# Performance work log

Measured on AMD Instinct MI355X. Metric: run time of the kernel, lower is better.

The kernel has to match this reference:

```python
import jax, jax.numpy as jnp
import numpy as np

N_FFT = 2048
HOP = 512
K = N_FFT // 2 + 1  # 1025 output frequency bins


def _dft_window_weights(n_fft):
    """Windowed real/imag DFT matrices, matching librosa hann (periodic) window
    and W[j,k] = exp(-2*pi*i*j*k/n_fft); conv weight = (W[:, :K] * win[:, None]).T."""
    n = np.arange(n_fft)
    win = 0.5 - 0.5 * np.cos(2.0 * np.pi * n / n_fft)  # hann, fftbins=True
    k = np.arange(n_fft // 2 + 1)
    ang = 2.0 * np.pi * np.outer(k, n) / n_fft  # (K, n_fft)
    w_real = np.cos(ang) * win[None, :]
    w_imag = -np.sin(ang) * win[None, :]
    return (jnp.asarray(w_real, jnp.float32), jnp.asarray(w_imag, jnp.float32))


def setup_inputs() -> dict:
    key = jax.random.key(0)
    x = jax.random.normal(key, (16, 2, 262144), dtype=jnp.float32)
    w_real, w_imag = _dft_window_weights(N_FFT)
    return {"x": x, "w_real": w_real, "w_imag": w_imag}


def reference(x, w_real, w_imag):
    B, C, L = x.shape
    pad = N_FFT // 2
    xp = jnp.pad(x, ((0, 0), (0, 0), (pad, pad)), mode="reflect")  # center=True
    T = (L + 2 * pad - N_FFT) // HOP + 1  # number of frames
    idx = HOP * jnp.arange(T)[:, None] + jnp.arange(N_FFT)[None, :]  # (T, n_fft)
    frames = xp[:, :, idx]  # (B, C, T, n_fft)
    # Windowed DFT as GEMM (same math as the conv-as-DFT in the torch module).
    real = jnp.einsum("bctn,kn->bckt", frames, w_real)  # (B, C, K, T)
    imag = jnp.einsum("bctn,kn->bckt", frames, w_imag)
    # torch.cat over channel dim -> (B, C*K, T), channel-major order
    real = real.reshape(B, C * K, T)
    imag = imag.reshape(B, C * K, T)
    return (real, imag)
```

## Files before the change

### kernel.cpp

```cpp
#include <hip/hip_runtime.h>
#include <hip/hip_fp16.h>

#define NFFT  2048
#define KF    1025
#define MROWS 2050
#define TT    513
#define HOPS  512
#define LSIG  262144
#define PADL  1024
#define XPADN 264192
#define XDN   66048
#define IMOFF (16 * MROWS * TT)
#define NBC   32

typedef __attribute__((ext_vector_type(8))) short bf16x8;
typedef __attribute__((ext_vector_type(4))) short bf16x4;
typedef __attribute__((ext_vector_type(4))) float f32x4;

__device__ __forceinline__ short f2bf(float f) {
    union { float f; unsigned u; } v; v.f = f;
    unsigned r = v.u + 0x7fffu + ((v.u >> 16) & 1u);
    return (short)(r >> 16);
}

typedef __attribute__((address_space(1))) void gas_void;
typedef __attribute__((address_space(3))) void las_void;

__device__ __forceinline__ void gload_lds16(const short* g, short* l) {
    __builtin_amdgcn_global_load_lds((gas_void*)(void*)const_cast<short*>(g),
                                     (las_void*)(void*)l, 16, 0, 0);
}

__global__ __launch_bounds__(256)
void prep_x(const float* __restrict__ x, short* __restrict__ xpad,
            short* __restrict__ xd) {
    const int bc = blockIdx.y;
    const int j4 = (blockIdx.x * 256 + threadIdx.x) * 4;
    const float* xb = x + (size_t)bc * LSIG;
    float4 v;
    if (j4 >= PADL && j4 + 4 <= PADL + LSIG) {
        v = *(const float4*)(xb + (j4 - PADL));
    } else {
        float t[4];
#pragma unroll
        for (int e = 0; e < 4; e++) {
            int s = j4 + e - PADL;
            if (s < 0) s = -s;
            if (s >= LSIG) s = 2 * LSIG - 2 - s;
            t[e] = xb[s];
        }
        v = make_float4(t[0], t[1], t[2], t[3]);
    }
    bf16x4 b = { f2bf(v.x), f2bf(v.y), f2bf(v.z), f2bf(v.w) };
    *(bf16x4*)(xpad + (size_t)bc * XPADN + j4) = b;
    const int j = j4 >> 2;
#pragma unroll
    for (int r = 0; r < 4; r++)
        xd[((size_t)r * NBC + bc) * XDN + j] = b[r];
}

__global__ __launch_bounds__(256)
void prep_basis(short* __restrict__ A) {
    const int r    = blockIdx.y;
    const int row  = blockIdx.x;
    const int kap  = row >> 1;
    const int reim = row & 1;
    for (int m = threadIdx.x; m < 512; m += 256) {
        float sv, cv;
        sincospif((float)(kap * m) * (1.0f / 256.0f), &sv, &cv);
        float win = 0.5f - 0.5f * cospif((float)(4 * m + r) * (1.0f / 1024.0f));
        float val = reim ? (-win * sv) : (win * cv);
        A[((size_t)r * 512 + row) * 512 + m] = f2bf(val);
    }
}

__global__ __launch_bounds__(256)
void stft_gemm_s(const short* __restrict__ Ab, const short* __restrict__ xd,
                 __half* __restrict__ S, int bc0) {
    __shared__ short As[128 * 64];
    __shared__ short Bs[128 * 64];

    const int tid   = threadIdx.x;
    const int bcl   = blockIdx.x;
    const int r     = blockIdx.y >> 2;
    const int mBase = (blockIdx.y & 3) * 128;
    const int t0    = blockIdx.z * 128;
    const short* Ap  = Ab + (size_t)r * 512 * 512;
    const short* xdp = xd + ((size_t)r * NBC + (bc0 + bcl)) * XDN;

    const int lane = tid & 63;
    const int wid  = tid >> 6;
    const int wm   = (wid >> 1) * 64;
    const int wn   = (wid & 1) * 64;
    const int l16  = lane & 15;
    const int quad = lane >> 4;

    const int lrow = lane >> 3;
    const int csrc = (lane & 7) ^ lrow;
    const int rb   = 32 * wid;

    const short* srcA[4]; const short* srcB[4];
    short* dstA[4]; short* dstB[4];
#pragma unroll
    for (int i = 0; i < 4; i++) {
        int rr = rb + 8 * i + lrow;
        srcA[i] = Ap  + (size_t)(mBase + rr) * 512 + csrc * 8;
        srcB[i] = xdp + (size_t)(t0 + rr) * 128 + csrc * 8;
        dstA[i] = As + (rb + 8 * i) * 64;
        dstB[i] = Bs + (rb + 8 * i) * 64;
    }

    f32x4 acc[4][4];
#pragma unroll
    for (int i = 0; i < 4; i++)
#pragma unroll
        for (int j = 0; j < 4; j++)
            acc[i][j] = (f32x4){0.f, 0.f, 0.f, 0.f};

    const int r7 = l16 & 7;
    for (int kt = 0; kt < 512; kt += 64) {
        __syncthreads();
#pragma unroll
        for (int i = 0; i < 4; i++) {
            gload_lds16(srcA[i] + kt, dstA[i]);
            gload_lds16(srcB[i] + kt, dstB[i]);
        }
        __syncthreads();
#pragma unroll
        for (int kk = 0; kk < 64; kk += 32) {
            const int p = ((kk >> 5) * 4 + quad) ^ r7;
            bf16x8 af[4], bfr[4];
#pragma unroll
            for (int i = 0; i < 4; i++)
                af[i] = *(const bf16x8*)(As + (wm + i * 16 + l16) * 64 + p * 8);
#pragma unroll
            for (int j = 0; j < 4; j++)
                bfr[j] = *(const bf16x8*)(Bs + (wn + j * 16 + l16) * 64 + p * 8);
#pragma unroll
            for (int i = 0; i < 4; i++)
#pragma unroll
                for (int j = 0; j < 4; j++)
                    acc[i][j] = __builtin_amdgcn_mfma_f32_16x16x32_bf16(
                        af[i], bfr[j], acc[i][j], 0, 0, 0);
        }
    }

    __half* Sb = S + ((size_t)bcl * 4 + r) * (512 * 512);
#pragma unroll
    for (int i = 0; i < 4; i++) {
#pragma unroll
        for (int rr = 0; rr < 4; rr++) {
            int row = mBase + wm + i * 16 + quad * 4 + rr;
            int tc  = t0 + wn + l16;
#pragma unroll
            for (int j = 0; j < 4; j++)
                Sb[(size_t)row * 512 + tc + j * 16] = __float2half(acc[i][j][rr]);
        }
    }
}

__global__ __launch_bounds__(256)
void stft_combine(const __half* __restrict__ S, float* __restrict__ out, int bc0) {
    const int kap = blockIdx.x;
    const int bcl = blockIdx.y;
    const int bcg = bc0 + bcl;
    float s1, c1;
    sincospif((float)kap * (1.0f / 1024.0f), &s1, &c1);
    const float cr1 = c1,               ci1 = -s1;
    const float cr2 = cr1*cr1 - ci1*ci1, ci2 = 2.f*cr1*ci1;
    const float cr3 = cr2*cr1 - ci2*ci1, ci3 = cr2*ci1 + ci2*cr1;
    const __half* Sb = S + (size_t)bcl * 4 * 512 * 512;
    float* oRe = out + (size_t)bcg * KF * TT;
    float* oIm = out + IMOFF + (size_t)bcg * KF * TT;

#pragma unroll
    for (int ti = 0; ti < 2; ti++) {
        const int t = threadIdx.x + ti * 256;
        float a[4], b[4];
#pragma unroll
        for (int r = 0; r < 4; r++) {
            a[r] = __half2float(Sb[((size_t)r * 512 + 2 * kap) * 512 + t]);
            b[r] = __half2float(Sb[((size_t)r * 512 + 2 * kap + 1) * 512 + t]);
        }
        const float u0 = a[0], v0 = b[0];
        const float u1 = cr1*a[1] - ci1*b[1], v1 = cr1*b[1] + ci1*a[1];
        const float u2 = cr2*a[2] - ci2*b[2], v2 = cr2*b[2] + ci2*a[2];
        const float u3 = cr3*a[3] - ci3*b[3], v3 = cr3*b[3] + ci3*a[3];
        oRe[(size_t)kap * TT + t]          = u0 + u1 + u2 + u3;
        oIm[(size_t)kap * TT + t]          = v0 + v1 + v2 + v3;
        oRe[(size_t)(kap + 512) * TT + t]  = u0 + v1 - u2 - v3;
        oIm[(size_t)(kap + 512) * TT + t]  = v0 - u1 - v2 + u3;
        oRe[(size_t)(512 - kap) * TT + t]  = u0 - v1 - u2 + v3;
        oIm[(size_t)(512 - kap) * TT + t]  = -(v0 + u1 - v2 - u3);
        oRe[(size_t)(1024 - kap) * TT + t] = u0 - u1 + u2 - u3;
        oIm[(size_t)(1024 - kap) * TT + t] = -(v0 - v1 + v2 - v3);
    }
}

__global__ __launch_bounds__(256)
void stft_tail(const float* __restrict__ wr, const float* __restrict__ wi,
               const short* __restrict__ xpad, float* __restrict__ out) {
    const int bx   = blockIdx.x;
    const int tid  = threadIdx.x;
    const int lane = tid & 63;
    const int wid  = tid >> 6;
    const int l16  = lane & 15;
    const int quad = lane >> 4;

    if (bx < 17) {
        const int mBase = bx * 128 + wid * 32;
        f32x4 acc[2][2];
#pragma unroll
        for (int i = 0; i < 2; i++)
#pragma unroll
            for (int j = 0; j < 2; j++) acc[i][j] = (f32x4){0.f,0.f,0.f,0.f};
        int ra0 = min(mBase + l16, MROWS - 1);
        int ra1 = min(mBase + 16 + l16, MROWS - 1);
        const float* a0p = ((ra0 < KF) ? (wr + (size_t)ra0 * NFFT)
                                       : (wi + (size_t)(ra0 - KF) * NFFT)) + quad * 8;
        const float* a1p = ((ra1 < KF) ? (wr + (size_t)ra1 * NFFT)
                                       : (wi + (size_t)(ra1 - KF) * NFFT)) + quad * 8;
        const short* b0p = xpad + (size_t)l16 * XPADN + LSIG + quad * 8;
        const short* b1p = b0p + (size_t)16 * XPADN;
        for (int kt = 0; kt < NFFT; kt += 32) {
            float4 f0 = *(const float4*)(a0p + kt), f1 = *(const float4*)(a0p + kt + 4);
            float4 g0 = *(const float4*)(a1p + kt), g1 = *(const float4*)(a1p + kt + 4);
            bf16x8 a0 = { f2bf(f0.x), f2bf(f0.y), f2bf(f0.z), f2bf(f0.w),
                          f2bf(f1.x), f2bf(f1.y), f2bf(f1.z), f2bf(f1.w) };
            bf16x8 a1 = { f2bf(g0.x), f2bf(g0.y), f2bf(g0.z), f2bf(g0.w),
                          f2bf(g1.x), f2bf(g1.y), f2bf(g1.z), f2bf(g1.w) };
            bf16x8 b0 = *(const bf16x8*)(b0p + kt);
            bf16x8 b1 = *(const bf16x8*)(b1p + kt);
            acc[0][0] = __builtin_amdgcn_mfma_f32_16x16x32_bf16(a0, b0, acc[0][0], 0,0,0);
            acc[0][1] = __builtin_amdgcn_mfma_f32_16x16x32_bf16(a0, b1, acc[0][1], 0,0,0);
            acc[1][0] = __builtin_amdgcn_mfma_f32_16x16x32_bf16(a1, b0, acc[1][0], 0,0,0);
            acc[1][1] = __builtin_amdgcn_mfma_f32_16x16x32_bf16(a1, b1, acc[1][1], 0,0,0);
        }
#pragma unroll
        for (int i = 0; i < 2; i++)
#pragma unroll
            for (int j = 0; j < 2; j++)
#pragma unroll
                for (int rr = 0; rr < 4; rr++) {
                    int row = mBase + i * 16 + quad * 4 + rr;
                    if (row >= MROWS) continue;
                    int bc = j * 16 + l16;
                    size_t o = (row < KF)
                        ? ((size_t)(bc * KF + row) * TT + (TT - 1))
                        : (IMOFF + (size_t)(bc * KF + (row - KF)) * TT + (TT - 1));
                    out[o] = acc[i][j][rr];
                }
    } else {
        const int idx = bx - 17;
        const int bc  = idx >> 3;
        const int tb  = idx & 7;
        const int t0  = (tb * 4 + wid) * 16;
        const int ls  = l16 & 3;
        const int k   = 256 + (ls & 1) * 512;
        const float* bp = ((ls & 2) ? wi : wr) + (size_t)k * NFFT + quad * 8;
        const short* ap = xpad + (size_t)bc * XPADN + (size_t)(t0 + l16) * HOPS + quad * 8;
        f32x4 acc0 = {0.f,0.f,0.f,0.f}, acc1 = {0.f,0.f,0.f,0.f};
        for (int kt = 0; kt < NFFT; kt += 64) {
            bf16x8 a0 = *(const bf16x8*)(ap + kt);
            bf16x8 a1 = *(const bf16x8*)(ap + kt + 32);
            float4 f0 = *(const float4*)(bp + kt), f1 = *(const float4*)(bp + kt + 4);
            float4 g0 = *(const float4*)(bp + kt + 32), g1 = *(const float4*)(bp + kt + 36);
            bf16x8 b0 = { f2bf(f0.x), f2bf(f0.y), f2bf(f0.z), f2bf(f0.w),
                          f2bf(f1.x), f2bf(f1.y), f2bf(f1.z), f2bf(f1.w) };
            bf16x8 b1 = { f2bf(g0.x), f2bf(g0.y), f2bf(g0.z), f2bf(g0.w),
                          f2bf(g1.x), f2bf(g1.y), f2bf(g1.z), f2bf(g1.w) };
            acc0 = __builtin_amdgcn_mfma_f32_16x16x32_bf16(a0, b0, acc0, 0,0,0);
            acc1 = __builtin_amdgcn_mfma_f32_16x16x32_bf16(a1, b1, acc1, 0,0,0);
        }
        if (l16 < 4) {
            size_t base = ((ls & 2) ? (size_t)IMOFF : 0) + (size_t)(bc * KF + k) * TT;
#pragma unroll
            for (int rr = 0; rr < 4; rr++) {
                int t = t0 + quad * 4 + rr;
                out[base + t] = acc0[rr] + acc1[rr];
            }
        }
    }
}

extern "C" void kernel_launch(void* const* d_in, const int* in_sizes, int n_in,
                              void* d_out, int out_size, void* d_ws, size_t ws_size,
                              hipStream_t stream) {
    const float* x  = (const float*)d_in[0];
    const float* wr = (const float*)d_in[1];
    const float* wi = (const float*)d_in[2];
    float* out = (float*)d_out;

    char* ws = (char*)d_ws;
    short*  xpad = (short*)ws;
    short*  xd   = (short*)(ws + 16908288);
    short*  Ab   = (short*)(ws + 33816576);
    __half* S    = (__half*)(ws + 35913728);

    const long long s_per_bc = 4LL * 512 * 512 * sizeof(__half);
    long long avail = (long long)ws_size - 35913728LL;
    int CH = (int)(avail / s_per_bc);
    if (CH < 1) CH = 1;
    if (CH > NBC) CH = NBC;

    prep_x<<<dim3(258, NBC), 256, 0, stream>>>(x, xpad, xd);
    prep_basis<<<dim3(512, 4), 256, 0, stream>>>(Ab);

    for (int bc0 = 0; bc0 < NBC; bc0 += CH) {
        int c = NBC - bc0 < CH ? NBC - bc0 : CH;
        stft_gemm_s<<<dim3(c, 16, 4), 256, 0, stream>>>(Ab, xd, S, bc0);
        stft_combine<<<dim3(256, c), 256, 0, stream>>>(S, out, bc0);
    }

    stft_tail<<<17 + 256, 256, 0, stream>>>(wr, wi, xpad, out);
}
```

Baseline: 321.2 us.

## Fuse radix-4 combine into GEMM epilogue, dropping fp16 intermediate buffer

The four polyphase sub-GEMMs are now computed in one kernel that keeps all four accumulator sets in registers. The radix-4 twiddle-free combine is applied in the epilogue, writing final fp32 outputs directly. This removes the fp16 S intermediate round trip through global memory, the separate combine kernel, and the chunking loop. The basis is now built from the provided weight tensors instead of sincos, and the last-frame tail is handled by extending the GEMM grid with clamped rows. In exchange the kernel uses more registers, with launch bounds set for 2 blocks per SM, and a smaller N tile, which may hurt reuse.

```diff
diff --git a/kernel.cpp b/kernel.cpp
--- a/kernel.cpp
+++ b/kernel.cpp
@@ -1,5 +1,4 @@
 #include <hip/hip_runtime.h>
-#include <hip/hip_fp16.h>
 
 #define NFFT  2048
 #define KF    1025
@@ -60,225 +59,165 @@
 }
 
 __global__ __launch_bounds__(256)
-void prep_basis(short* __restrict__ A) {
-    const int r    = blockIdx.y;
-    const int row  = blockIdx.x;
-    const int kap  = row >> 1;
-    const int reim = row & 1;
-    for (int m = threadIdx.x; m < 512; m += 256) {
-        float sv, cv;
-        sincospif((float)(kap * m) * (1.0f / 256.0f), &sv, &cv);
-        float win = 0.5f - 0.5f * cospif((float)(4 * m + r) * (1.0f / 1024.0f));
-        float val = reim ? (-win * sv) : (win * cv);
-        A[((size_t)r * 512 + row) * 512 + m] = f2bf(val);
-    }
-}
-
-__global__ __launch_bounds__(256)
-void stft_gemm_s(const short* __restrict__ Ab, const short* __restrict__ xd,
-                 __half* __restrict__ S, int bc0) {
-    __shared__ short As[128 * 64];
-    __shared__ short Bs[128 * 64];
+void prep_basis2(const float* __restrict__ wr, const float* __restrict__ wi,
+                 short* __restrict__ A) {
+    const int r   = blockIdx.y;
+    const int row = blockIdx.x;
+    const float* w = ((row & 1) ? wi : wr) + (size_t)(row >> 1) * NFFT + r;
+    short* dst = A + ((size_t)r * 512 + row) * 512;
+    for (int m = threadIdx.x; m < 512; m += 256)
+        dst[m] = f2bf(w[4 * m]);
+}
+
+__global__ __launch_bounds__(256, 2)
+void stft_gemm_f(const short* __restrict__ Ab, const short* __restrict__ xd,
+                 float* __restrict__ out) {
+    __shared__ short As[2][128 * 64];
+    __shared__ short Bs[2][64 * 64];
 
     const int tid   = threadIdx.x;
-    const int bcl   = blockIdx.x;
-    const int r     = blockIdx.y >> 2;
-    const int mBase = (blockIdx.y & 3) * 128;
-    const int t0    = blockIdx.z * 128;
-    const short* Ap  = Ab + (size_t)r * 512 * 512;
-    const short* xdp = xd + ((size_t)r * NBC + (bc0 + bcl)) * XDN;
+    const int bcg   = blockIdx.x;
+    const int mBase = blockIdx.y * 128;
+    const int t0    = blockIdx.z * 64;
 
     const int lane = tid & 63;
     const int wid  = tid >> 6;
     const int wm   = (wid >> 1) * 64;
-    const int wn   = (wid & 1) * 64;
+    const int wn   = (wid & 1) * 32;
     const int l16  = lane & 15;
     const int quad = lane >> 4;
 
     const int lrow = lane >> 3;
     const int csrc = (lane & 7) ^ lrow;
-    const int rb   = 32 * wid;
-
-    const short* srcA[4]; const short* srcB[4];
-    short* dstA[4]; short* dstB[4];
-#pragma unroll
-    for (int i = 0; i < 4; i++) {
-        int rr = rb + 8 * i + lrow;
-        srcA[i] = Ap  + (size_t)(mBase + rr) * 512 + csrc * 8;
-        srcB[i] = xdp + (size_t)(t0 + rr) * 128 + csrc * 8;
-        dstA[i] = As + (rb + 8 * i) * 64;
-        dstB[i] = Bs + (rb + 8 * i) * 64;
-    }
-
-    f32x4 acc[4][4];
-#pragma unroll
-    for (int i = 0; i < 4; i++)
-#pragma unroll
-        for (int j = 0; j < 4; j++)
-            acc[i][j] = (f32x4){0.f, 0.f, 0.f, 0.f};
+    const int rbA  = 32 * wid;
+    const int rbB  = 16 * wid;
+
+    int br0 = t0 + rbB + lrow;       if (br0 > 515) br0 = 515;
+    int br1 = t0 + rbB + 8 + lrow;   if (br1 > 515) br1 = 515;
+
+    f32x4 acc[4][4][2];
+#pragma unroll
+    for (int r = 0; r < 4; r++)
+#pragma unroll
+        for (int i = 0; i < 4; i++)
+#pragma unroll
+            for (int j = 0; j < 2; j++)
+                acc[r][i][j] = (f32x4){0.f, 0.f, 0.f, 0.f};
 
     const int r7 = l16 & 7;
-    for (int kt = 0; kt < 512; kt += 64) {
-        __syncthreads();
+
+#pragma unroll
+    for (int rp = 0; rp < 2; rp++) {
+        const short* Ap0 = Ab + ((size_t)(2 * rp) * 512 + mBase + rbA + lrow) * 512 + csrc * 8;
+        const short* Ap1 = Ap0 + (size_t)512 * 512;
+        const short* Bbase0 = xd + ((size_t)(2 * rp) * NBC + bcg) * XDN + csrc * 8;
+        const short* Bbase1 = Bbase0 + (size_t)NBC * XDN;
+
+        for (int kt = 0; kt < 512; kt += 64) {
+            __syncthreads();
+#pragma unroll
+            for (int i = 0; i < 4; i++) {
+                gload_lds16(Ap0 + i * (8 * 512) + kt, &As[0][(rbA + 8 * i) * 64]);
+                gload_lds16(Ap1 + i * (8 * 512) + kt, &As[1][(rbA + 8 * i) * 64]);
+            }
+            gload_lds16(Bbase0 + (size_t)br0 * 128 + kt, &Bs[0][(rbB + 0) * 64]);
+            gload_lds16(Bbase0 + (size_t)br1 * 128 + kt, &Bs[0][(rbB + 8) * 64]);
+            gload_lds16(Bbase1 + (size_t)br0 * 128 + kt, &Bs[1][(rbB + 0) * 64]);
+            gload_lds16(Bbase1 + (size_t)br1 * 128 + kt, &Bs[1][(rbB + 8) * 64]);
+            __syncthreads();
+#pragma unroll
+            for (int rr2 = 0; rr2 < 2; rr2++) {
+#pragma unroll
+                for (int kk = 0; kk < 64; kk += 32) {
+                    const int p = ((kk >> 5) * 4 + quad) ^ r7;
+                    bf16x8 af[4], bfr[2];
+#pragma unroll
+                    for (int i = 0; i < 4; i++)
+                        af[i] = *(const bf16x8*)(&As[rr2][(wm + i * 16 + l16) * 64 + p * 8]);
+#pragma unroll
+                    for (int j = 0; j < 2; j++)
+                        bfr[j] = *(const bf16x8*)(&Bs[rr2][(wn + j * 16 + l16) * 64 + p * 8]);
+#pragma unroll
+                    for (int i = 0; i < 4; i++)
+#pragma unroll
+                        for (int j = 0; j < 2; j++)
+                            acc[2 * rp + rr2][i][j] = __builtin_amdgcn_mfma_f32_16x16x32_bf16(
+                                af[i], bfr[j], acc[2 * rp + rr2][i][j], 0, 0, 0);
+                }
+            }
+        }
+    }
+
+    float* oRe = out + (size_t)bcg * KF * TT;
+    float* oIm = out + (size_t)IMOFF + (size_t)bcg * KF * TT;
+
+#pragma unroll
+    for (int j = 0; j < 2; j++) {
+        const int t = t0 + wn + j * 16 + l16;
+        if (t >= TT) continue;
 #pragma unroll
         for (int i = 0; i < 4; i++) {
-            gload_lds16(srcA[i] + kt, dstA[i]);
-            gload_lds16(srcB[i] + kt, dstB[i]);
-        }
-        __syncthreads();
-#pragma unroll
-        for (int kk = 0; kk < 64; kk += 32) {
-            const int p = ((kk >> 5) * 4 + quad) ^ r7;
-            bf16x8 af[4], bfr[4];
-#pragma unroll
-            for (int i = 0; i < 4; i++)
-                af[i] = *(const bf16x8*)(As + (wm + i * 16 + l16) * 64 + p * 8);
-#pragma unroll
-            for (int j = 0; j < 4; j++)
-                bfr[j] = *(const bf16x8*)(Bs + (wn + j * 16 + l16) * 64 + p * 8);
-#pragma unroll
-            for (int i = 0; i < 4; i++)
-#pragma unroll
-                for (int j = 0; j < 4; j++)
-                    acc[i][j] = __builtin_amdgcn_mfma_f32_16x16x32_bf16(
-                        af[i], bfr[j], acc[i][j], 0, 0, 0);
-        }
-    }
-
-    __half* Sb = S + ((size_t)bcl * 4 + r) * (512 * 512);
-#pragma unroll
-    for (int i = 0; i < 4; i++) {
-#pragma unroll
-        for (int rr = 0; rr < 4; rr++) {
-            int row = mBase + wm + i * 16 + quad * 4 + rr;
-            int tc  = t0 + wn + l16;
-#pragma unroll
-            for (int j = 0; j < 4; j++)
-                Sb[(size_t)row * 512 + tc + j * 16] = __float2half(acc[i][j][rr]);
-        }
-    }
-}
-
-__global__ __launch_bounds__(256)
-void stft_combine(const __half* __restrict__ S, float* __restrict__ out, int bc0) {
-    const int kap = blockIdx.x;
-    const int bcl = blockIdx.y;
-    const int bcg = bc0 + bcl;
-    float s1, c1;
-    sincospif((float)kap * (1.0f / 1024.0f), &s1, &c1);
-    const float cr1 = c1,               ci1 = -s1;
-    const float cr2 = cr1*cr1 - ci1*ci1, ci2 = 2.f*cr1*ci1;
-    const float cr3 = cr2*cr1 - ci2*ci1, ci3 = cr2*ci1 + ci2*cr1;
-    const __half* Sb = S + (size_t)bcl * 4 * 512 * 512;
-    float* oRe = out + (size_t)bcg * KF * TT;
-    float* oIm = out + IMOFF + (size_t)bcg * KF * TT;
-
-#pragma unroll
-    for (int ti = 0; ti < 2; ti++) {
-        const int t = threadIdx.x + ti * 256;
-        float a[4], b[4];
-#pragma unroll
-        for (int r = 0; r < 4; r++) {
-            a[r] = __half2float(Sb[((size_t)r * 512 + 2 * kap) * 512 + t]);
-            b[r] = __half2float(Sb[((size_t)r * 512 + 2 * kap + 1) * 512 + t]);
-        }
-        const float u0 = a[0], v0 = b[0];
-        const float u1 = cr1*a[1] - ci1*b[1], v1 = cr1*b[1] + ci1*a[1];
-        const float u2 = cr2*a[2] - ci2*b[2], v2 = cr2*b[2] + ci2*a[2];
-        const float u3 = cr3*a[3] - ci3*b[3], v3 = cr3*b[3] + ci3*a[3];
-        oRe[(size_t)kap * TT + t]          = u0 + u1 + u2 + u3;
-        oIm[(size_t)kap * TT + t]          = v0 + v1 + v2 + v3;
-        oRe[(size_t)(kap + 512) * TT + t]  = u0 + v1 - u2 - v3;
-        oIm[(size_t)(kap + 512) * TT + t]  = v0 - u1 - v2 + u3;
-        oRe[(size_t)(512 - kap) * TT + t]  = u0 - v1 - u2 + v3;
-        oIm[(size_t)(512 - kap) * TT + t]  = -(v0 + u1 - v2 - u3);
-        oRe[(size_t)(1024 - kap) * TT + t] = u0 - u1 + u2 - u3;
-        oIm[(size_t)(1024 - kap) * TT + t] = -(v0 - v1 + v2 - v3);
+            const int rowb = mBase + wm + i * 16 + quad * 4;
+#pragma unroll
+            for (int h = 0; h < 2; h++) {
+                const int kap = (rowb >> 1) + h;
+                const float u0 = acc[0][i][j][2 * h], v0 = acc[0][i][j][2 * h + 1];
+                const float u1 = acc[1][i][j][2 * h], v1 = acc[1][i][j][2 * h + 1];
+                const float u2 = acc[2][i][j][2 * h], v2 = acc[2][i][j][2 * h + 1];
+                const float u3 = acc[3][i][j][2 * h], v3 = acc[3][i][j][2 * h + 1];
+                const float Eu = u0 + u2, Epu = u0 - u2;
+                const float Ou = u1 + u3, Opu = u1 - u3;
+                const float Ev = v0 + v2, Epv = v0 - v2;
+                const float Ov = v1 + v3, Opv = v1 - v3;
+                const size_t rA = (size_t)kap * TT + t;
+                const size_t rB = (size_t)(kap + 512) * TT + t;
+                const size_t rC = (size_t)(512 - kap) * TT + t;
+                const size_t rD = (size_t)(1024 - kap) * TT + t;
+                oRe[rA] = Eu + Ou;    oIm[rA] = Ev + Ov;
+                oRe[rB] = Epu + Opv;  oIm[rB] = Epv - Opu;
+                oRe[rC] = Epu - Opv;  oIm[rC] = -(Epv + Opu);
+                oRe[rD] = Eu - Ou;    oIm[rD] = -(Ev - Ov);
+            }
+        }
     }
 }
 
 __global__ __launch_bounds__(256)
 void stft_tail(const float* __restrict__ wr, const float* __restrict__ wi,
                const short* __restrict__ xpad, float* __restrict__ out) {
-    const int bx   = blockIdx.x;
-    const int tid  = threadIdx.x;
+    const int tb  = blockIdx.x;
+    const int bc  = blockIdx.y;
+    const int tid = threadIdx.x;
     const int lane = tid & 63;
     const int wid  = tid >> 6;
     const int l16  = lane & 15;
     const int quad = lane >> 4;
 
-    if (bx < 17) {
-        const int mBase = bx * 128 + wid * 32;
-        f32x4 acc[2][2];
-#pragma unroll
-        for (int i = 0; i < 2; i++)
-#pragma unroll
-            for (int j = 0; j < 2; j++) acc[i][j] = (f32x4){0.f,0.f,0.f,0.f};
-        int ra0 = min(mBase + l16, MROWS - 1);
-        int ra1 = min(mBase + 16 + l16, MROWS - 1);
-        const float* a0p = ((ra0 < KF) ? (wr + (size_t)ra0 * NFFT)
-                                       : (wi + (size_t)(ra0 - KF) * NFFT)) + quad * 8;
-        const float* a1p = ((ra1 < KF) ? (wr + (size_t)ra1 * NFFT)
-                                       : (wi + (size_t)(ra1 - KF) * NFFT)) + quad * 8;
-        const short* b0p = xpad + (size_t)l16 * XPADN + LSIG + quad * 8;
-        const short* b1p = b0p + (size_t)16 * XPADN;
-        for (int kt = 0; kt < NFFT; kt += 32) {
-            float4 f0 = *(const float4*)(a0p + kt), f1 = *(const float4*)(a0p + kt + 4);
-            float4 g0 = *(const float4*)(a1p + kt), g1 = *(const float4*)(a1p + kt + 4);
-            bf16x8 a0 = { f2bf(f0.x), f2bf(f0.y), f2bf(f0.z), f2bf(f0.w),
-                          f2bf(f1.x), f2bf(f1.y), f2bf(f1.z), f2bf(f1.w) };
-            bf16x8 a1 = { f2bf(g0.x), f2bf(g0.y), f2bf(g0.z), f2bf(g0.w),
-                          f2bf(g1.x), f2bf(g1.y), f2bf(g1.z), f2bf(g1.w) };
-            bf16x8 b0 = *(const bf16x8*)(b0p + kt);
-            bf16x8 b1 = *(const bf16x8*)(b1p + kt);
-            acc[0][0] = __builtin_amdgcn_mfma_f32_16x16x32_bf16(a0, b0, acc[0][0], 0,0,0);
-            acc[0][1] = __builtin_amdgcn_mfma_f32_16x16x32_bf16(a0, b1, acc[0][1], 0,0,0);
-            acc[1][0] = __builtin_amdgcn_mfma_f32_16x16x32_bf16(a1, b0, acc[1][0], 0,0,0);
-            acc[1][1] = __builtin_amdgcn_mfma_f32_16x16x32_bf16(a1, b1, acc[1][1], 0,0,0);
-        }
-#pragma unroll
-        for (int i = 0; i < 2; i++)
-#pragma unroll
-            for (int j = 0; j < 2; j++)
-#pragma unroll
-                for (int rr = 0; rr < 4; rr++) {
-                    int row = mBase + i * 16 + quad * 4 + rr;
-                    if (row >= MROWS) continue;
-                    int bc = j * 16 + l16;
-                    size_t o = (row < KF)
-                        ? ((size_t)(bc * KF + row) * TT + (TT - 1))
-                        : (IMOFF + (size_t)(bc * KF + (row - KF)) * TT + (TT - 1));
-                    out[o] = acc[i][j][rr];
-                }
-    } else {
-        const int idx = bx - 17;
-        const int bc  = idx >> 3;
-        const int tb  = idx & 7;
-        const int t0  = (tb * 4 + wid) * 16;
-        const int ls  = l16 & 3;
-        const int k   = 256 + (ls & 1) * 512;
-        const float* bp = ((ls & 2) ? wi : wr) + (size_t)k * NFFT + quad * 8;
-        const short* ap = xpad + (size_t)bc * XPADN + (size_t)(t0 + l16) * HOPS + quad * 8;
-        f32x4 acc0 = {0.f,0.f,0.f,0.f}, acc1 = {0.f,0.f,0.f,0.f};
-        for (int kt = 0; kt < NFFT; kt += 64) {
-            bf16x8 a0 = *(const bf16x8*)(ap + kt);
-            bf16x8 a1 = *(const bf16x8*)(ap + kt + 32);
-            float4 f0 = *(const float4*)(bp + kt), f1 = *(const float4*)(bp + kt + 4);
-            float4 g0 = *(const float4*)(bp + kt + 32), g1 = *(const float4*)(bp + kt + 36);
-            bf16x8 b0 = { f2bf(f0.x), f2bf(f0.y), f2bf(f0.z), f2bf(f0.w),
-                          f2bf(f1.x), f2bf(f1.y), f2bf(f1.z), f2bf(f1.w) };
-            bf16x8 b1 = { f2bf(g0.x), f2bf(g0.y), f2bf(g0.z), f2bf(g0.w),
-                          f2bf(g1.x), f2bf(g1.y), f2bf(g1.z), f2bf(g1.w) };
-            acc0 = __builtin_amdgcn_mfma_f32_16x16x32_bf16(a0, b0, acc0, 0,0,0);
-            acc1 = __builtin_amdgcn_mfma_f32_16x16x32_bf16(a1, b1, acc1, 0,0,0);
-        }
-        if (l16 < 4) {
-            size_t base = ((ls & 2) ? (size_t)IMOFF : 0) + (size_t)(bc * KF + k) * TT;
-#pragma unroll
-            for (int rr = 0; rr < 4; rr++) {
-                int t = t0 + quad * 4 + rr;
-                out[base + t] = acc0[rr] + acc1[rr];
-            }
+    const int t0 = (tb * 4 + wid) * 16;
+    const int ls = l16 & 3;
+    const int k  = 256 + (ls & 1) * 512;
+    const float* bp = ((ls & 2) ? wi : wr) + (size_t)k * NFFT + quad * 8;
+    const int tr = min(t0 + l16, 512);
+    const short* ap = xpad + (size_t)bc * XPADN + (size_t)tr * HOPS + quad * 8;
+    f32x4 acc0 = {0.f, 0.f, 0.f, 0.f}, acc1 = {0.f, 0.f, 0.f, 0.f};
+    for (int kt = 0; kt < NFFT; kt += 64) {
+        bf16x8 a0 = *(const bf16x8*)(ap + kt);
+        bf16x8 a1 = *(const bf16x8*)(ap + kt + 32);
+        float4 f0 = *(const float4*)(bp + kt), f1 = *(const float4*)(bp + kt + 4);
+        float4 g0 = *(const float4*)(bp + kt + 32), g1 = *(const float4*)(bp + kt + 36);
+        bf16x8 b0 = { f2bf(f0.x), f2bf(f0.y), f2bf(f0.z), f2bf(f0.w),
+                      f2bf(f1.x), f2bf(f1.y), f2bf(f1.z), f2bf(f1.w) };
+        bf16x8 b1 = { f2bf(g0.x), f2bf(g0.y), f2bf(g0.z), f2bf(g0.w),
+                      f2bf(g1.x), f2bf(g1.y), f2bf(g1.z), f2bf(g1.w) };
+        acc0 = __builtin_amdgcn_mfma_f32_16x16x32_bf16(a0, b0, acc0, 0, 0, 0);
+        acc1 = __builtin_amdgcn_mfma_f32_16x16x32_bf16(a1, b1, acc1, 0, 0, 0);
+    }
+    if (l16 < 4) {
+        size_t base = ((ls & 2) ? (size_t)IMOFF : 0) + (size_t)(bc * KF + k) * TT;
+#pragma unroll
+        for (int rr = 0; rr < 4; rr++) {
+            int t = t0 + quad * 4 + rr;
+            if (t < TT) out[base + t] = acc0[rr] + acc1[rr];
         }
     }
 }
@@ -292,25 +231,12 @@
     float* out = (float*)d_out;
 
     char* ws = (char*)d_ws;
-    short*  xpad = (short*)ws;
-    short*  xd   = (short*)(ws + 16908288);
-    short*  Ab   = (short*)(ws + 33816576);
-    __half* S    = (__half*)(ws + 35913728);
-
-    const long long s_per_bc = 4LL * 512 * 512 * sizeof(__half);
-    long long avail = (long long)ws_size - 35913728LL;
-    int CH = (int)(avail / s_per_bc);
-    if (CH < 1) CH = 1;
-    if (CH > NBC) CH = NBC;
+    short* xpad = (short*)ws;
+    short* xd   = (short*)(ws + 16908288);
+    short* Ab   = (short*)(ws + 33816576);
 
     prep_x<<<dim3(258, NBC), 256, 0, stream>>>(x, xpad, xd);
-    prep_basis<<<dim3(512, 4), 256, 0, stream>>>(Ab);
-
-    for (int bc0 = 0; bc0 < NBC; bc0 += CH) {
-        int c = NBC - bc0 < CH ? NBC - bc0 : CH;
-        stft_gemm_s<<<dim3(c, 16, 4), 256, 0, stream>>>(Ab, xd, S, bc0);
-        stft_combine<<<dim3(256, c), 256, 0, stream>>>(S, out, bc0);
-    }
-
-    stft_tail<<<17 + 256, 256, 0, stream>>>(wr, wi, xpad, out);
-}
+    prep_basis2<<<dim3(512, 4), 256, 0, stream>>>(wr, wi, Ab);
+    stft_gemm_f<<<dim3(NBC, 4, 9), 256, 0, stream>>>(Ab, xd, out);
+    stft_tail<<<dim3(9, NBC), 256, 0, stream>>>(wr, wi, xpad, out);
+}
```

Measured after the change: 315.5 us. No clear change (-1.8%).
